# Performance work log

Measured on AMD Instinct MI355X. Metric: run time of the kernel, lower is better.

Reference implementation:

```python
import jax, jax.numpy as jnp
import numpy as np

B, S, H, D = 4, 2048, 16, 128
E = H * D  # emb_dim = 2048


def setup_inputs() -> dict:
    key = jax.random.key(0)
    ks = jax.random.split(key, 9)
    s_in = 1.0 / np.sqrt(E)
    return {
        "inputs": jax.random.normal(ks[0], (B, S, E), dtype=jnp.float32),
        "Wq": jax.random.normal(ks[1], (E, E), dtype=jnp.float32) * s_in,
        "bq": jnp.zeros((E,), dtype=jnp.float32),
        "Wk": jax.random.normal(ks[2], (E, E), dtype=jnp.float32) * s_in,
        "bk": jnp.zeros((E,), dtype=jnp.float32),
        "Wv": jax.random.normal(ks[3], (E, E), dtype=jnp.float32) * s_in,
        "bv": jnp.zeros((E,), dtype=jnp.float32),
        "Wo": jax.random.normal(ks[4], (E, E), dtype=jnp.float32) * s_in,
        "bo": jnp.zeros((E,), dtype=jnp.float32),
    }


def reference(inputs, Wq, bq, Wk, bk, Wv, bv, Wo, bo):
    b, s, e = inputs.shape
    # QKV projections -> [B, H, S, D]
    q = (inputs @ Wq + bq).reshape(b, s, H, D).transpose(0, 2, 1, 3)
    k = (inputs @ Wk + bk).reshape(b, s, H, D).transpose(0, 2, 1, 3)
    v = (inputs @ Wv + bv).reshape(b, s, H, D).transpose(0, 2, 1, 3)
    scale = 1.0 / jnp.sqrt(jnp.asarray(D, dtype=q.dtype))
    # Scaled dot-product attention (what the blockwise flash loop computes)
    scores = jnp.einsum('bhqd,bhkd->bhqk', q, k) * scale
    probs = jax.nn.softmax(scores, axis=-1)
    attn = jnp.einsum('bhqk,bhkd->bhqd', probs, v)
    attn = attn.transpose(0, 2, 1, 3).reshape(b, s, e)
    return attn @ Wo + bo
```

## Files before the change

### kernel.cpp

```cpp
#include <hip/hip_runtime.h>
#include <hip/hip_bf16.h>
#include <stdint.h>

typedef __bf16 bf16;
typedef float f32x4 __attribute__((ext_vector_type(4)));
typedef bf16 bf16x4 __attribute__((ext_vector_type(4)));
typedef bf16 bf16x8 __attribute__((ext_vector_type(8)));

#define DEV __device__ __forceinline__

DEV void gload16(const void* g, void* l) {
  __builtin_amdgcn_global_load_lds((const __attribute__((address_space(1))) void*)g,
                                   (__attribute__((address_space(3))) void*)l, 16, 0, 0);
}

DEV f32x4 mfma16(bf16x8 a, bf16x8 b, f32x4 c) {
  return __builtin_amdgcn_mfma_f32_16x16x32_bf16(a, b, c, 0, 0, 0);
}

#if __has_builtin(__builtin_amdgcn_exp2f)
DEV float EXP2F(float x) { return __builtin_amdgcn_exp2f(x); }
#else
DEV float EXP2F(float x) { return exp2f(x); }
#endif

static constexpr int Bn = 4, Sn = 2048, Hn = 16, Dn = 128, En = 2048, Mn = 8192;

__global__ void cvt_x(const float* __restrict__ in, bf16* __restrict__ out, int n8) {
  int i = blockIdx.x * blockDim.x + threadIdx.x;
  int stride = gridDim.x * blockDim.x;
  for (int idx = i; idx < n8; idx += stride) {
    const float4* p = (const float4*)(in + (size_t)idx * 8);
    float4 a = p[0], b = p[1];
    bf16x8 o;
    o[0]=(bf16)a.x; o[1]=(bf16)a.y; o[2]=(bf16)a.z; o[3]=(bf16)a.w;
    o[4]=(bf16)b.x; o[5]=(bf16)b.y; o[6]=(bf16)b.z; o[7]=(bf16)b.w;
    *(bf16x8*)(out + (size_t)idx * 8) = o;
  }
}

__global__ void wtrans(const float* __restrict__ W, bf16* __restrict__ Wt) {
  __shared__ bf16 t[64][65];
  int tx = threadIdx.x & 15, ty = threadIdx.x >> 4;
  int c0 = blockIdx.x * 64, r0 = blockIdx.y * 64;
  #pragma unroll
  for (int i = 0; i < 4; ++i) {
    int r = i * 16 + ty;
    float4 v = *(const float4*)&W[(size_t)(r0 + r) * En + c0 + tx * 4];
    t[r][tx*4+0] = (bf16)v.x; t[r][tx*4+1] = (bf16)v.y;
    t[r][tx*4+2] = (bf16)v.z; t[r][tx*4+3] = (bf16)v.w;
  }
  __syncthreads();
  #pragma unroll
  for (int i = 0; i < 4; ++i) {
    int c = i * 16 + ty;
    bf16x4 o;
    #pragma unroll
    for (int j = 0; j < 4; ++j) o[j] = t[tx*4+j][c];
    *(bf16x4*)&Wt[(size_t)(c0 + c) * En + r0 + tx * 4] = o;
  }
}

__global__ void vtrans(const bf16* __restrict__ V, bf16* __restrict__ Vt) {
  __shared__ bf16 t[64][65];
  int tx = threadIdx.x & 15, ty = threadIdx.x >> 4;
  int s0 = blockIdx.x * 64, d0 = blockIdx.y * 64, bh = blockIdx.z;
  const bf16* Vi = V + (size_t)bh * Sn * Dn;
  bf16* Vo = Vt + (size_t)bh * Sn * Dn;
  #pragma unroll
  for (int i = 0; i < 4; ++i) {
    int r = i * 16 + ty;
    bf16x4 v = *(const bf16x4*)&Vi[(size_t)(s0 + r) * Dn + d0 + tx * 4];
    #pragma unroll
    for (int j = 0; j < 4; ++j) t[r][tx*4+j] = v[j];
  }
  __syncthreads();
  #pragma unroll
  for (int i = 0; i < 4; ++i) {
    int dd = i * 16 + ty;
    bf16x4 o;
    #pragma unroll
    for (int j = 0; j < 4; ++j) o[j] = t[tx*4+j][dd];
    *(bf16x4*)&Vo[(size_t)(d0 + dd) * Sn + s0 + tx * 4] = o;
  }
}

template<int OUT_MODE>
__global__ __launch_bounds__(256, 2) void gemm_bt(
    const bf16* __restrict__ A, const bf16* __restrict__ Bt,
    const float* __restrict__ bias, void* __restrict__ Cout,
    int M, int N, int K)
{
  __shared__ __align__(16) uint8_t smem[32768];
  uint8_t* As = smem;
  uint8_t* Bs = smem + 16384;
  const int tid = threadIdx.x;
  const int lane = tid & 63, w = tid >> 6;
  const int wm = w >> 1, wn = w & 1;
  const int g = lane >> 4, lr = lane & 15;
  const int mbase = blockIdx.y * 128, nbase = blockIdx.x * 128;

  f32x4 acc[4][4] = {};

  const int nkt = K >> 6;
  for (int kt = 0; kt < nkt; ++kt) {
    const bf16* Ag = A + (size_t)mbase * K + kt * 64;
    const bf16* Bg = Bt + (size_t)nbase * K + kt * 64;
    #pragma unroll
    for (int it = 0; it < 4; ++it) {
      int cl = it * 256 + tid;
      int row = cl >> 3, cs = cl & 7;
      int cg = cs ^ (row & 7);
      int ldsoff = (it * 256 + (tid & ~63)) * 16;
      gload16(Ag + (size_t)row * K + cg * 8, As + ldsoff);
      gload16(Bg + (size_t)row * K + cg * 8, Bs + ldsoff);
    }
    __syncthreads();
    #pragma unroll
    for (int ks = 0; ks < 2; ++ks) {
      bf16x8 af[4], bfm[4];
      #pragma unroll
      for (int mf = 0; mf < 4; ++mf) {
        int row = wm * 64 + mf * 16 + lr;
        af[mf] = *(const bf16x8*)(As + row * 128 + (((ks * 4 + g) ^ (row & 7)) << 4));
      }
      #pragma unroll
      for (int nf = 0; nf < 4; ++nf) {
        int row = wn * 64 + nf * 16 + lr;
        bfm[nf] = *(const bf16x8*)(Bs + row * 128 + (((ks * 4 + g) ^ (row & 7)) << 4));
      }
      #pragma unroll
      for (int mf = 0; mf < 4; ++mf)
        #pragma unroll
        for (int nf = 0; nf < 4; ++nf)
          acc[mf][nf] = mfma16(af[mf], bfm[nf], acc[mf][nf]);
    }
    __syncthreads();
  }

  #pragma unroll
  for (int mf = 0; mf < 4; ++mf) {
    #pragma unroll
    for (int nf = 0; nf < 4; ++nf) {
      int n = nbase + wn * 64 + nf * 16 + lr;
      float bv = bias[n];
      #pragma unroll
      for (int r = 0; r < 4; ++r) {
        int m = mbase + wm * 64 + mf * 16 + g * 4 + r;
        float val = acc[mf][nf][r] + bv;
        if constexpr (OUT_MODE == 0) {
          int b = m >> 11, s = m & 2047, h = n >> 7, d = n & 127;
          ((bf16*)Cout)[((size_t)(b * Hn + h) * Sn + s) * Dn + d] = (bf16)val;
        } else {
          ((float*)Cout)[(size_t)m * N + n] = val;
        }
      }
    }
  }
}

__global__ __launch_bounds__(256, 2) void attn(
    const bf16* __restrict__ Q, const bf16* __restrict__ K,
    const bf16* __restrict__ Vt, bf16* __restrict__ O)
{
  __shared__ __align__(16) uint8_t smem[65536];
  const int tid = threadIdx.x, lane = tid & 63, w = tid >> 6;
  const int g = lane >> 4, lr = lane & 15;
  const int lid = blockIdx.x + (int)gridDim.x * blockIdx.y;
  const int xcd = lid & 7, j = lid >> 3;
  const int bh = xcd * 8 + (j >> 4);
  const int q0 = (j & 15) * 128;
  const size_t hoff = (size_t)bh * Sn * Dn;
  const bf16* Qh = Q + hoff;
  const bf16* Kh = K + hoff;
  const bf16* Vh = Vt + hoff;
  const float SC2 = 0.12751744f;

  #pragma unroll
  for (int it = 0; it < 8; ++it) {
    int cl = it * 256 + tid;
    int row = cl >> 4, cs = cl & 15;
    int cg = cs ^ (row & 7);
    gload16(Qh + (size_t)(q0 + row) * Dn + cg * 8, smem + (it * 256 + (tid & ~63)) * 16);
  }
  __syncthreads();
  bf16x8 qf[2][4];
  #pragma unroll
  for (int nf = 0; nf < 2; ++nf)
    #pragma unroll
    for (int ks = 0; ks < 4; ++ks) {
      int row = w * 32 + nf * 16 + lr;
      qf[nf][ks] = *(const bf16x8*)(smem + row * 256 + (((ks * 4 + g) ^ (row & 7)) << 4));
    }
  __syncthreads();

  const int vd = tid >> 1, vhw = tid & 1;
  const bf16* vrow = Vh + (size_t)vd * Sn + vhw * 32;

  uint4 vr0, vr1, vr2, vr3;
  #pragma unroll
  for (int it = 0; it < 4; ++it) {
    int cl = it * 256 + tid;
    int row = cl >> 4, cs = cl & 15;
    int cg = cs ^ (row & 7);
    gload16(Kh + (size_t)row * Dn + cg * 8, smem + (it * 256 + (tid & ~63)) * 16);
  }
  { const uint4* vs = (const uint4*)vrow;
    vr0 = vs[0]; vr1 = vs[1]; vr2 = vs[2]; vr3 = vs[3]; }

  f32x4 o[2][8] = {};
  float m2[2] = { -__builtin_inff(), -__builtin_inff() };
  float lrun[2] = { 0.f, 0.f };

  for (int t = 0; t < 32; ++t) {
    const int cur = t & 1;
    uint8_t* Kcur = smem + (cur << 14);
    uint8_t* Knxt = smem + ((cur ^ 1) << 14);
    uint8_t* Vcur = smem + 32768 + (cur << 14);
    asm volatile("s_waitcnt vmcnt(0)" ::: "memory");
    {
      uint8_t* base = Vcur + vd * 128;
      const int sw = vd & 7, cb = vhw * 4;
      *(uint4*)(base + (((cb + 0) ^ sw) << 4)) = make_uint4(vr0.x, vr0.y, vr2.x, vr2.y);
      *(uint4*)(base + (((cb + 1) ^ sw) << 4)) = make_uint4(vr0.z, vr0.w, vr2.z, vr2.w);
      *(uint4*)(base + (((cb + 2) ^ sw) << 4)) = make_uint4(vr1.x, vr1.y, vr3.x, vr3.y);
      *(uint4*)(base + (((cb + 3) ^ sw) << 4)) = make_uint4(vr1.z, vr1.w, vr3.z, vr3.w);
    }
    if (t < 31) {
      const int kvn = (t + 1) * 64;
      #pragma unroll
      for (int it = 0; it < 4; ++it) {
        int cl = it * 256 + tid;
        int row = cl >> 4, cs = cl & 15;
        int cg = cs ^ (row & 7);
        gload16(Kh + (size_t)(kvn + row) * Dn + cg * 8,
                Knxt + (it * 256 + (tid & ~63)) * 16);
      }
      const uint4* vs = (const uint4*)(vrow + kvn);
      vr0 = vs[0]; vr1 = vs[1]; vr2 = vs[2]; vr3 = vs[3];
    }
    asm volatile("s_waitcnt lgkmcnt(0)" ::: "memory");
    asm volatile("s_barrier" ::: "memory");

    f32x4 sfr[2][4] = {};
    __builtin_amdgcn_s_setprio(1);
    #pragma unroll
    for (int ks = 0; ks < 4; ++ks) {
      #pragma unroll
      for (int mf = 0; mf < 4; ++mf) {
        int row = mf * 16 + lr;
        bf16x8 kf = *(const bf16x8*)(Kcur + row * 256 + (((ks * 4 + g) ^ (row & 7)) << 4));
        sfr[0][mf] = mfma16(kf, qf[0][ks], sfr[0][mf]);
        sfr[1][mf] = mfma16(kf, qf[1][ks], sfr[1][mf]);
      }
    }
    __builtin_amdgcn_s_setprio(0);

    bf16x8 pa[2][2];
    #pragma unroll
    for (int nf = 0; nf < 2; ++nf) {
      f32x4 a0, a1;
      #pragma unroll
      for (int r = 0; r < 4; ++r) a0[r] = fmaxf(sfr[nf][0][r], sfr[nf][1][r]);
      #pragma unroll
      for (int r = 0; r < 4; ++r) a1[r] = fmaxf(sfr[nf][2][r], sfr[nf][3][r]);
      #pragma unroll
      for (int r = 0; r < 4; ++r) a0[r] = fmaxf(a0[r], a1[r]);
      float mx = fmaxf(fmaxf(a0[0], a0[1]), fmaxf(a0[2], a0[3]));
      mx = fmaxf(mx, __shfl_xor(mx, 16));
      mx = fmaxf(mx, __shfl_xor(mx, 32));
      float pm2 = mx * SC2;
      if (__any(pm2 > m2[nf] + 8.f)) {
        float mnew = fmaxf(m2[nf], pm2);
        float fsc = EXP2F(m2[nf] - mnew);
        m2[nf] = mnew;
        lrun[nf] *= fsc;
        float fv[4];
        #pragma unroll
        for (int r = 0; r < 4; ++r) fv[r] = __shfl(fsc, g * 4 + r);
        #pragma unroll
        for (int df = 0; df < 8; ++df)
          #pragma unroll
          for (int r = 0; r < 4; ++r) o[nf][df][r] *= fv[r];
      }
      const float mc = m2[nf];
      f32x4 p[4];
      #pragma unroll
      for (int mf = 0; mf < 4; ++mf)
        #pragma unroll
        for (int r = 0; r < 4; ++r)
          p[mf][r] = EXP2F(__builtin_fmaf(sfr[nf][mf][r], SC2, -mc));
      f32x4 s0, s1;
      #pragma unroll
      for (int r = 0; r < 4; ++r) s0[r] = p[0][r] + p[1][r];
      #pragma unroll
      for (int r = 0; r < 4; ++r) s1[r] = p[2][r] + p[3][r];
      #pragma unroll
      for (int r = 0; r < 4; ++r) s0[r] += s1[r];
      float ps = (s0[0] + s0[1]) + (s0[2] + s0[3]);
      ps += __shfl_xor(ps, 16);
      ps += __shfl_xor(ps, 32);
      lrun[nf] += ps;
      #pragma unroll
      for (int ks = 0; ks < 2; ++ks) {
        bf16x8 tt;
        #pragma unroll
        for (int i = 0; i < 4; ++i) {
          tt[i]     = (bf16)p[2 * ks][i];
          tt[i + 4] = (bf16)p[2 * ks + 1][i];
        }
        pa[nf][ks] = tt;
      }
    }

    __builtin_amdgcn_s_setprio(1);
    #pragma unroll
    for (int ks = 0; ks < 2; ++ks) {
      #pragma unroll
      for (int df = 0; df < 8; ++df) {
        int row = df * 16 + lr;
        bf16x8 vf = *(const bf16x8*)(Vcur + row * 128 + (((ks * 4 + g) ^ (row & 7)) << 4));
        o[0][df] = mfma16(pa[0][ks], vf, o[0][df]);
        o[1][df] = mfma16(pa[1][ks], vf, o[1][df]);
      }
    }
    __builtin_amdgcn_s_setprio(0);
    asm volatile("s_barrier" ::: "memory");
  }

  const int b = bh >> 4, h = bh & 15;
  #pragma unroll
  for (int nf = 0; nf < 2; ++nf) {
    float inv = 1.f / lrun[nf];
    float iv[4];
    #pragma unroll
    for (int r = 0; r < 4; ++r) iv[r] = __shfl(inv, g * 4 + r);
    #pragma unroll
    for (int df = 0; df < 8; ++df) {
      #pragma unroll
      for (int r = 0; r < 4; ++r) {
        int qrow = q0 + w * 32 + nf * 16 + g * 4 + r;
        int d = df * 16 + lr;
        size_t m = (size_t)b * Sn + qrow;
        O[m * En + h * Dn + d] = (bf16)(o[nf][df][r] * iv[r]);
      }
    }
  }
}

extern "C" void kernel_launch(void* const* d_in, const int* in_sizes, int n_in,
                              void* d_out, int out_size, void* d_ws, size_t ws_size,
                              hipStream_t stream) {
  const float* X  = (const float*)d_in[0];
  const float* Wq = (const float*)d_in[1];
  const float* bq = (const float*)d_in[2];
  const float* Wk = (const float*)d_in[3];
  const float* bk = (const float*)d_in[4];
  const float* Wv = (const float*)d_in[5];
  const float* bv = (const float*)d_in[6];
  const float* Wo = (const float*)d_in[7];
  const float* bo = (const float*)d_in[8];

  bf16* ws = (bf16*)d_ws;
  const size_t szE = (size_t)Mn * En;
  const size_t szW = (size_t)En * En;
  bf16* Xb  = ws;
  bf16* Wqt = Xb + szE;
  bf16* Wkt = Wqt + szW;
  bf16* Wvt = Wkt + szW;
  bf16* Wot = Wvt + szW;
  bf16* Qb  = Wot + szW;
  bf16* Kb  = Qb + szE;
  bf16* Vb  = Kb + szE;
  bf16* Vtp = Vb + szE;
  bf16* AO  = Vb;

  cvt_x<<<2048, 256, 0, stream>>>(X, Xb, (int)(szE / 8));
  wtrans<<<dim3(32, 32), 256, 0, stream>>>(Wq, Wqt);
  wtrans<<<dim3(32, 32), 256, 0, stream>>>(Wk, Wkt);
  wtrans<<<dim3(32, 32), 256, 0, stream>>>(Wv, Wvt);
  wtrans<<<dim3(32, 32), 256, 0, stream>>>(Wo, Wot);
  gemm_bt<0><<<dim3(16, 64), 256, 0, stream>>>(Xb, Wqt, bq, Qb, Mn, En, En);
  gemm_bt<0><<<dim3(16, 64), 256, 0, stream>>>(Xb, Wkt, bk, Kb, Mn, En, En);
  gemm_bt<0><<<dim3(16, 64), 256, 0, stream>>>(Xb, Wvt, bv, Vb, Mn, En, En);
  vtrans<<<dim3(32, 2, 64), 256, 0, stream>>>(Vb, Vtp);
  attn<<<dim3(16, 64), 256, 0, stream>>>(Qb, Kb, Vtp, AO);
  gemm_bt<1><<<dim3(16, 64), 256, 0, stream>>>(AO, Wot, bo, d_out, Mn, En, En);
}
```

Baseline: 509.3 us.

## Replace 128x128 GEMM with double-buffered 256x256 tile kernel and fuse QKV projections

Swaps the single-buffered 128x128 GEMM for a 512-thread 256x256 tile kernel. It double-buffers LDS with interleaved async global-to-LDS staging, raises MFMA priority with setprio, and uses XCD-aware block swizzling. Q, K and V projections become one GEMM over the contiguous transposed weights (N = 3E), with bias and output selected per tile. The goal is more data reuse per tile, latency hiding and fewer launches. In exchange it needs 128KB of LDS and many barriers, and it depends on Wqt/Wkt/Wvt and Qb/Kb/Vb being contiguous in the workspace.

Measured after the change: 505.9 us. No clear change (-0.7%).

```diff
diff --git a/kernel.cpp b/kernel.cpp
--- a/kernel.cpp
+++ b/kernel.cpp
@@ -85,72 +85,144 @@
   }
 }
 
+#define STAGE_A(H, DBUF, KTN) do { \
+    const bf16* s_ = A + (size_t)(mbase + (tid >> 2)) * K + (KTN) * 64 + (H) * 32 + (tid & 3) * 8; \
+    uint8_t* d_ = (DBUF) + (H) * 16384 + (w << 10); \
+    gload16(s_, d_); \
+    gload16(s_ + (size_t)128 * K, d_ + 8192); \
+  } while (0)
+#define STAGE_B(H, DBUF, KTN) do { \
+    const bf16* s_ = Bt + (size_t)(nbase + (tid >> 2)) * K + (KTN) * 64 + (H) * 32 + (tid & 3) * 8; \
+    uint8_t* d_ = (DBUF) + (H) * 16384 + (w << 10); \
+    gload16(s_, d_); \
+    gload16(s_ + (size_t)128 * K, d_ + 8192); \
+  } while (0)
+
 template<int OUT_MODE>
-__global__ __launch_bounds__(256, 2) void gemm_bt(
+__global__ __launch_bounds__(512, 2) void gemm256(
     const bf16* __restrict__ A, const bf16* __restrict__ Bt,
-    const float* __restrict__ bias, void* __restrict__ Cout,
-    int M, int N, int K)
+    const float* __restrict__ b0, const float* __restrict__ b1,
+    const float* __restrict__ b2, void* __restrict__ Cout,
+    int M, int N, int K, int nbx)
 {
-  __shared__ __align__(16) uint8_t smem[32768];
-  uint8_t* As = smem;
-  uint8_t* Bs = smem + 16384;
-  const int tid = threadIdx.x;
-  const int lane = tid & 63, w = tid >> 6;
-  const int wm = w >> 1, wn = w & 1;
+  __shared__ __align__(16) uint8_t smem[131072];
+  const int tid = threadIdx.x, lane = tid & 63, w = tid >> 6;
+  const int wm = w >> 2, wn = w & 3;
   const int g = lane >> 4, lr = lane & 15;
-  const int mbase = blockIdx.y * 128, nbase = blockIdx.x * 128;
-
-  f32x4 acc[4][4] = {};
-
-  const int nkt = K >> 6;
-  for (int kt = 0; kt < nkt; ++kt) {
-    const bf16* Ag = A + (size_t)mbase * K + kt * 64;
-    const bf16* Bg = Bt + (size_t)nbase * K + kt * 64;
-    #pragma unroll
-    for (int it = 0; it < 4; ++it) {
-      int cl = it * 256 + tid;
-      int row = cl >> 3, cs = cl & 7;
-      int cg = cs ^ (row & 7);
-      int ldsoff = (it * 256 + (tid & ~63)) * 16;
-      gload16(Ag + (size_t)row * K + cg * 8, As + ldsoff);
-      gload16(Bg + (size_t)row * K + cg * 8, Bs + ldsoff);
-    }
-    __syncthreads();
-    #pragma unroll
-    for (int ks = 0; ks < 2; ++ks) {
-      bf16x8 af[4], bfm[4];
-      #pragma unroll
-      for (int mf = 0; mf < 4; ++mf) {
-        int row = wm * 64 + mf * 16 + lr;
-        af[mf] = *(const bf16x8*)(As + row * 128 + (((ks * 4 + g) ^ (row & 7)) << 4));
-      }
-      #pragma unroll
-      for (int nf = 0; nf < 4; ++nf) {
-        int row = wn * 64 + nf * 16 + lr;
-        bfm[nf] = *(const bf16x8*)(Bs + row * 128 + (((ks * 4 + g) ^ (row & 7)) << 4));
-      }
-      #pragma unroll
-      for (int mf = 0; mf < 4; ++mf)
-        #pragma unroll
-        for (int nf = 0; nf < 4; ++nf)
-          acc[mf][nf] = mfma16(af[mf], bfm[nf], acc[mf][nf]);
-    }
-    __syncthreads();
-  }
-
-  #pragma unroll
-  for (int mf = 0; mf < 4; ++mf) {
-    #pragma unroll
-    for (int nf = 0; nf < 4; ++nf) {
-      int n = nbase + wn * 64 + nf * 16 + lr;
-      float bv = bias[n];
+  const int lid = blockIdx.x;
+  const int swz = (lid & 7) * ((int)gridDim.x >> 3) + (lid >> 3);
+  const int bx = swz % nbx, by = swz / nbx;
+  const int mbase = by * 256, nbase = bx * 256;
+
+  f32x4 acc[8][4] = {};
+
+  STAGE_A(0, smem, 0);
+  STAGE_B(0, smem + 65536, 0);
+  STAGE_A(1, smem, 0);
+  STAGE_B(1, smem + 65536, 0);
+  asm volatile("s_waitcnt vmcnt(0)" ::: "memory");
+  __builtin_amdgcn_s_barrier();
+
+  const int NKT = K >> 6;
+  for (int kt = 0; kt < NKT; ++kt) {
+    const int cur = kt & 1;
+    uint8_t* Acur = smem + (cur << 15);
+    uint8_t* Bcur = smem + 65536 + (cur << 15);
+    uint8_t* Anxt = smem + ((cur ^ 1) << 15);
+    uint8_t* Bnxt = smem + 65536 + ((cur ^ 1) << 15);
+    const bool notlast = (kt + 1 < NKT);
+    bf16x8 af[8], bfr0, bfr1;
+
+    asm volatile("s_waitcnt vmcnt(4)" ::: "memory");
+    #pragma unroll
+    for (int mf = 0; mf < 8; ++mf)
+      af[mf] = *(const bf16x8*)(Acur + (wm * 128 + mf * 16 + lr) * 64 + g * 16);
+    bfr0 = *(const bf16x8*)(Bcur + (wn * 64 +  0 + lr) * 64 + g * 16);
+    bfr1 = *(const bf16x8*)(Bcur + (wn * 64 + 16 + lr) * 64 + g * 16);
+    if (notlast) STAGE_A(0, Anxt, kt + 1);
+    __builtin_amdgcn_s_barrier();
+    asm volatile("s_waitcnt lgkmcnt(0)" ::: "memory");
+    __builtin_amdgcn_sched_barrier(0);
+    __builtin_amdgcn_s_setprio(1);
+    #pragma unroll
+    for (int mf = 0; mf < 8; ++mf) {
+      acc[mf][0] = mfma16(af[mf], bfr0, acc[mf][0]);
+      acc[mf][1] = mfma16(af[mf], bfr1, acc[mf][1]);
+    }
+    __builtin_amdgcn_s_setprio(0);
+    __builtin_amdgcn_s_barrier();
+
+    bfr0 = *(const bf16x8*)(Bcur + (wn * 64 + 32 + lr) * 64 + g * 16);
+    bfr1 = *(const bf16x8*)(Bcur + (wn * 64 + 48 + lr) * 64 + g * 16);
+    if (notlast) STAGE_B(0, Bnxt, kt + 1);
+    __builtin_amdgcn_s_barrier();
+    asm volatile("s_waitcnt lgkmcnt(0)" ::: "memory");
+    __builtin_amdgcn_sched_barrier(0);
+    __builtin_amdgcn_s_setprio(1);
+    #pragma unroll
+    for (int mf = 0; mf < 8; ++mf) {
+      acc[mf][2] = mfma16(af[mf], bfr0, acc[mf][2]);
+      acc[mf][3] = mfma16(af[mf], bfr1, acc[mf][3]);
+    }
+    __builtin_amdgcn_s_setprio(0);
+    __builtin_amdgcn_s_barrier();
+
+    if (notlast) { asm volatile("s_waitcnt vmcnt(4)" ::: "memory"); }
+    else         { asm volatile("s_waitcnt vmcnt(0)" ::: "memory"); }
+    #pragma unroll
+    for (int mf = 0; mf < 8; ++mf)
+      af[mf] = *(const bf16x8*)(Acur + 16384 + (wm * 128 + mf * 16 + lr) * 64 + g * 16);
+    bfr0 = *(const bf16x8*)(Bcur + 16384 + (wn * 64 +  0 + lr) * 64 + g * 16);
+    bfr1 = *(const bf16x8*)(Bcur + 16384 + (wn * 64 + 16 + lr) * 64 + g * 16);
+    if (notlast) STAGE_A(1, Anxt, kt + 1);
+    __builtin_amdgcn_s_barrier();
+    asm volatile("s_waitcnt lgkmcnt(0)" ::: "memory");
+    __builtin_amdgcn_sched_barrier(0);
+    __builtin_amdgcn_s_setprio(1);
+    #pragma unroll
+    for (int mf = 0; mf < 8; ++mf) {
+      acc[mf][0] = mfma16(af[mf], bfr0, acc[mf][0]);
+      acc[mf][1] = mfma16(af[mf], bfr1, acc[mf][1]);
+    }
+    __builtin_amdgcn_s_setprio(0);
+    __builtin_amdgcn_s_barrier();
+
+    bfr0 = *(const bf16x8*)(Bcur + 16384 + (wn * 64 + 32 + lr) * 64 + g * 16);
+    bfr1 = *(const bf16x8*)(Bcur + 16384 + (wn * 64 + 48 + lr) * 64 + g * 16);
+    if (notlast) STAGE_B(1, Bnxt, kt + 1);
+    __builtin_amdgcn_s_barrier();
+    asm volatile("s_waitcnt lgkmcnt(0)" ::: "memory");
+    __builtin_amdgcn_sched_barrier(0);
+    __builtin_amdgcn_s_setprio(1);
+    #pragma unroll
+    for (int mf = 0; mf < 8; ++mf) {
+      acc[mf][2] = mfma16(af[mf], bfr0, acc[mf][2]);
+      acc[mf][3] = mfma16(af[mf], bfr1, acc[mf][3]);
+    }
+    __builtin_amdgcn_s_setprio(0);
+    __builtin_amdgcn_s_barrier();
+  }
+
+  int tsel = 0;
+  const float* bsel = b0;
+  if constexpr (OUT_MODE == 0) {
+    tsel = nbase >> 11;
+    bsel = (tsel == 0) ? b0 : ((tsel == 1) ? b1 : b2);
+  }
+  #pragma unroll
+  for (int j = 0; j < 4; ++j) {
+    int n = nbase + wn * 64 + j * 16 + lr;
+    float bv = (OUT_MODE == 0) ? bsel[n & 2047] : bsel[n];
+    #pragma unroll
+    for (int mf = 0; mf < 8; ++mf) {
       #pragma unroll
       for (int r = 0; r < 4; ++r) {
-        int m = mbase + wm * 64 + mf * 16 + g * 4 + r;
-        float val = acc[mf][nf][r] + bv;
+        int m = mbase + wm * 128 + mf * 16 + g * 4 + r;
+        float val = acc[mf][j][r] + bv;
         if constexpr (OUT_MODE == 0) {
-          int b = m >> 11, s = m & 2047, h = n >> 7, d = n & 127;
-          ((bf16*)Cout)[((size_t)(b * Hn + h) * Sn + s) * Dn + d] = (bf16)val;
+          int b = m >> 11, s = m & 2047, nn = n & 2047, h = nn >> 7, d = nn & 127;
+          ((bf16*)Cout)[(size_t)tsel * ((size_t)Mn * En) +
+                        ((size_t)(b * Hn + h) * Sn + s) * Dn + d] = (bf16)val;
         } else {
           ((float*)Cout)[(size_t)m * N + n] = val;
         }
@@ -380,10 +452,8 @@
   wtrans<<<dim3(32, 32), 256, 0, stream>>>(Wk, Wkt);
   wtrans<<<dim3(32, 32), 256, 0, stream>>>(Wv, Wvt);
   wtrans<<<dim3(32, 32), 256, 0, stream>>>(Wo, Wot);
-  gemm_bt<0><<<dim3(16, 64), 256, 0, stream>>>(Xb, Wqt, bq, Qb, Mn, En, En);
-  gemm_bt<0><<<dim3(16, 64), 256, 0, stream>>>(Xb, Wkt, bk, Kb, Mn, En, En);
-  gemm_bt<0><<<dim3(16, 64), 256, 0, stream>>>(Xb, Wvt, bv, Vb, Mn, En, En);
+  gemm256<0><<<768, 512, 0, stream>>>(Xb, Wqt, bq, bk, bv, Qb, Mn, 3 * En, En, 24);
   vtrans<<<dim3(32, 2, 64), 256, 0, stream>>>(Vb, Vtp);
   attn<<<dim3(16, 64), 256, 0, stream>>>(Qb, Kb, Vtp, AO);
-  gemm_bt<1><<<dim3(16, 64), 256, 0, stream>>>(AO, Wot, bo, d_out, Mn, En, En);
-}
+  gemm256<1><<<256, 512, 0, stream>>>(AO, Wot, bo, nullptr, nullptr, d_out, Mn, En, En, 8);
+}
```
